# Kernel optimization log

Hardware: AMD Instinct MI355X
Metric: run time of the kernel (lower is better)

Reference implementation:

```python
import jax, jax.numpy as jnp
import numpy as np

GRID_SIZE, SPLINE_ORDER = 5, 3
NUM_BASES = GRID_SIZE + SPLINE_ORDER  # 8
GRID = jnp.asarray(np.arange(-SPLINE_ORDER, GRID_SIZE + SPLINE_ORDER + 1, dtype=np.float32) * (2.0 / GRID_SIZE) - 1.0)  # (12,)


def _b_splines(x):
    # x: (M, F) -> (M, F, NUM_BASES), Cox-de Boor recursion on shared uniform grid
    g = GRID
    xe = x[..., None]
    b = ((xe >= g[:-1]) & (xe < g[1:])).astype(x.dtype)
    for k in range(1, SPLINE_ORDER + 1):
        b = ((xe - g[:-(k + 1)]) / (g[k:-1] - g[:-(k + 1)]) * b[..., :-1]
             + (g[k + 1:] - xe) / (g[k + 1:] - g[1:-k]) * b[..., 1:])
    return b


def _kan_linear(x, base_w, spline_w):
    # x: (M, Fin); base_w: (Fout, Fin); spline_w: (Fout, Fin, NUM_BASES)
    base = jax.nn.silu(x) @ base_w.T
    spl = _b_splines(x).reshape(x.shape[0], -1) @ spline_w.reshape(spline_w.shape[0], -1).T
    return base + spl


def _ln(x, g, b, eps=1e-5):
    mu = jnp.mean(x, -1, keepdims=True)
    var = jnp.var(x, -1, keepdims=True)
    return (x - mu) * jax.lax.rsqrt(var + eps) * g + b


def _dwconv(img, w, b):
    C = img.shape[1]
    out = jax.lax.conv_general_dilated(img, w, (1, 1), 'SAME',
        dimension_numbers=('NCHW', 'OIHW', 'NCHW'), feature_group_count=C)
    return out + b[None, :, None, None]


def _dw_bn_relu(x, H, W, w, b, gamma, beta, eps=1e-5):
    # BN in eval mode with running_mean=0, running_var=1
    B, N, C = x.shape
    img = x.transpose(0, 2, 1).reshape(B, C, H, W)
    out = _dwconv(img, w, b)
    out = out * (gamma * (1.0 / np.sqrt(1.0 + eps)))[None, :, None, None] + beta[None, :, None, None]
    out = jax.nn.relu(out)
    return out.reshape(B, C, H * W).transpose(0, 2, 1)


def _cross_selective_scan(img, x_proj_w, dt_w, dt_b, A_logs, Ds, g, b):
    # img: (B, Di, H, W). 4-direction diagonal/antidiagonal selective scan (VMamba-style).
    B, Di, H, W = img.shape
    L = H * W
    K = x_proj_w.shape[0]
    R = dt_w.shape[2]
    Nst = A_logs.shape[1]
    i = jnp.arange(H)[:, None]
    j = jnp.arange(W)[None, :]
    diag = (i + j) % W
    adiag = (j - i) % W
    diag_inv = (jnp.arange(W)[None, :] - i) % W
    adiag_inv = (jnp.arange(W)[None, :] + i) % W

    def gather(x, idx):
        gth = jnp.take_along_axis(x, idx[None, None], axis=3)  # (B,Di,H,W)
        return gth.transpose(0, 1, 3, 2).reshape(B, Di, L)

    def scatter(flat, idx_inv):
        v = flat.reshape(B, Di, W, H).transpose(0, 1, 3, 2)
        return jnp.take_along_axis(v, idx_inv[None, None], axis=3)

    gd, gad = gather(img, diag), gather(img, adiag)
    xs = jnp.stack([gd, gad, jnp.flip(gd, -1), jnp.flip(gad, -1)], axis=1)  # (B,K,Di,L)
    x_dbl = jnp.einsum('bkdl,kcd->bkcl', xs, x_proj_w)
    dts, Bs, Cs = jnp.split(x_dbl, [R, R + Nst], axis=2)  # (B,K,R,L),(B,K,N,L),(B,K,N,L)
    dts = jnp.einsum('bkrl,kdr->bkdl', dts, dt_w)
    delta = jax.nn.softplus(dts + dt_b[None, :, :, None])  # (B,K,Di,L)
    A = -jnp.exp(A_logs).reshape(K, Di, Nst)

    def step(hst, inp):
        u_t, d_t, B_t, C_t = inp  # (B,K,Di),(B,K,Di),(B,K,N),(B,K,N)
        dA = jnp.exp(d_t[..., None] * A)
        hst = dA * hst + (d_t * u_t)[..., None] * B_t[:, :, None, :]
        return hst, jnp.einsum('bkdn,bkn->bkd', hst, C_t)

    h0 = jnp.zeros((B, K, Di, Nst), img.dtype)
    _, ys = jax.lax.scan(step, h0,
        (xs.transpose(3, 0, 1, 2), delta.transpose(3, 0, 1, 2),
         Bs.transpose(3, 0, 1, 2), Cs.transpose(3, 0, 1, 2)))  # ys: (L,B,K,Di)
    ys = ys.transpose(1, 2, 3, 0) + Ds.reshape(K, Di)[None, :, :, None] * xs  # (B,K,Di,L)
    yd = ys[:, 0] + jnp.flip(ys[:, 2], -1)
    ya = ys[:, 1] + jnp.flip(ys[:, 3], -1)
    y = scatter(yd, diag_inv) + scatter(ya, adiag_inv)  # (B,Di,H,W)
    y = y.reshape(B, Di, L).transpose(0, 2, 1)
    return _ln(y, g, b)  # (B,L,Di)


def setup_inputs():
    key = jax.random.key(0)
    ks = iter(jax.random.split(key, 48))
    B, H, W, C = 4, 64, 64, 96
    Di, K, Nst = 2 * C, 4, 16
    R = int(np.ceil(C / 16))
    L = H * W

    def rn(shape, s=0.05):
        return jax.random.normal(next(ks), shape, jnp.float32) * s

    return dict(
        x=jax.random.normal(next(ks), (B, L, C), jnp.float32),
        H=H, W=W,
        norm1_g=jnp.ones((C,), jnp.float32), norm1_b=jnp.zeros((C,), jnp.float32),
        in_proj_w=rn((2 * Di, C)),
        conv_w=rn((Di, 1, 3, 3), 0.2), conv_b=jnp.zeros((Di,), jnp.float32),
        x_proj_w=rn((K, R + 2 * Nst, Di)),
        dt_w=rn((K, Di, R), 0.1), dt_b=rn((K, Di), 0.1),
        A_logs=jax.random.uniform(next(ks), (K * Di, Nst), jnp.float32),
        Ds=jnp.ones((K * Di,), jnp.float32),
        out_norm_g=jnp.ones((Di,), jnp.float32), out_norm_b=jnp.zeros((Di,), jnp.float32),
        out_proj_w=rn((C, Di)),
        norm2_g=jnp.ones((C,), jnp.float32), norm2_b=jnp.zeros((C,), jnp.float32),
        fc1_base_w=rn((C, C)), fc1_spline_w=rn((C, C, NUM_BASES), 0.02),
        fc2_base_w=rn((C, C)), fc2_spline_w=rn((C, C, NUM_BASES), 0.02),
        fc3_base_w=rn((C, C)), fc3_spline_w=rn((C, C, NUM_BASES), 0.02),
        dw1_w=rn((C, 1, 3, 3), 0.2), dw1_b=jnp.zeros((C,), jnp.float32),
        dw1_g=jnp.ones((C,), jnp.float32), dw1_beta=jnp.zeros((C,), jnp.float32),
        dw2_w=rn((C, 1, 3, 3), 0.2), dw2_b=jnp.zeros((C,), jnp.float32),
        dw2_g=jnp.ones((C,), jnp.float32), dw2_beta=jnp.zeros((C,), jnp.float32),
        dw3_w=rn((C, 1, 3, 3), 0.2), dw3_b=jnp.zeros((C,), jnp.float32),
        dw3_g=jnp.ones((C,), jnp.float32), dw3_beta=jnp.zeros((C,), jnp.float32),
    )


def reference(x, H, W, norm1_g, norm1_b, in_proj_w, conv_w, conv_b, x_proj_w,
              dt_w, dt_b, A_logs, Ds, out_norm_g, out_norm_b, out_proj_w,
              norm2_g, norm2_b, fc1_base_w, fc1_spline_w, fc2_base_w, fc2_spline_w,
              fc3_base_w, fc3_spline_w, dw1_w, dw1_b, dw1_g, dw1_beta,
              dw2_w, dw2_b, dw2_g, dw2_beta, dw3_w, dw3_b, dw3_g, dw3_beta):
    B, L, C = x.shape
    # --- SS2D branch ---
    h = _ln(x, norm1_g, norm1_b)
    xz = h @ in_proj_w.T  # (B,L,2*Di)
    Di = xz.shape[-1] // 2
    xin, z = xz[..., :Di], xz[..., Di:]
    img = xin.transpose(0, 2, 1).reshape(B, Di, H, W)
    img = jax.nn.silu(_dwconv(img, conv_w, conv_b))
    y = _cross_selective_scan(img, x_proj_w, dt_w, dt_b, A_logs, Ds, out_norm_g, out_norm_b)
    y = y * jax.nn.silu(z)
    x = x + y @ out_proj_w.T
    # --- KAN branch ---
    h = _ln(x, norm2_g, norm2_b)
    M = B * L
    t = _kan_linear(h.reshape(M, C), fc1_base_w, fc1_spline_w).reshape(B, L, -1)
    t = _dw_bn_relu(t, H, W, dw1_w, dw1_b, dw1_g, dw1_beta)
    t = _kan_linear(t.reshape(M, -1), fc2_base_w, fc2_spline_w).reshape(B, L, -1)
    t = _dw_bn_relu(t, H, W, dw2_w, dw2_b, dw2_g, dw2_beta)
    t = _kan_linear(t.reshape(M, -1), fc3_base_w, fc3_spline_w).reshape(B, L, -1)
    t = _dw_bn_relu(t, H, W, dw3_w, dw3_b, dw3_g, dw3_beta)
    return x + t
```

## Files before the change

### kernel.cpp

```cpp
#include <hip/hip_runtime.h>
#include <math.h>

constexpr int B_  = 4;
constexpr int H_  = 64;
constexpr int W_  = 64;
constexpr int C_  = 96;
constexpr int L_  = H_ * W_;
constexpr int DI  = 192;
constexpr int K_  = 4;
constexpr int NST = 16;
constexpr int R_  = 6;
constexpr int M_  = B_ * L_;

constexpr int NCH = 128;
constexpr int CL  = 32;
constexpr int DG  = 12;

constexpr int KANK = 864;
constexpr int KLAY = 96 * KANK;

typedef __attribute__((ext_vector_type(8))) short short8;
typedef __attribute__((ext_vector_type(4))) float floatx4;
typedef __attribute__((ext_vector_type(4))) unsigned short ushort4v;

__device__ __forceinline__ float wave_sum64(float v) {
#pragma unroll
  for (int off = 1; off < 64; off <<= 1) v += __shfl_xor(v, off, 64);
  return v;
}

__device__ __forceinline__ float exp2_hw(float x) {
  return __builtin_amdgcn_exp2f(x);
}

__device__ __forceinline__ int pos_kl(int k, int l) {
  int ll = (k >= 2) ? (L_ - 1 - l) : l;
  int i = ll & 63;
  int j = ll >> 6;
  int col = ((k & 1) == 0) ? ((i + j) & 63) : ((j - i) & 63);
  return (i << 6) + col;
}

__device__ __forceinline__ int pos_pair(int pr, int ll) {
  int i = ll & 63, j = ll >> 6;
  int col = (pr == 0) ? ((i + j) & 63) : ((j - i) & 63);
  return (i << 6) + col;
}

__device__ __forceinline__ float silu_f(float x) {
  return x / (1.f + __expf(-x));
}

__device__ __forceinline__ float softplus_fast(float s) {
  return fmaxf(s, 0.f) + __logf(1.f + __expf(-fabsf(s)));
}

__device__ __forceinline__ unsigned short f2bf(float f) {
  unsigned u = __float_as_uint(f);
  unsigned r = (u + 0x7FFFu + ((u >> 16) & 1u)) >> 16;
  return (unsigned short)r;
}

__device__ __forceinline__ float bf2f(unsigned short h) {
  return __uint_as_float(((unsigned)h) << 16);
}

__device__ __forceinline__ void spline8(float x, float* bb ) {
#pragma unroll
  for (int i2 = 0; i2 < 11; i2++) {
    float g0 = 0.4f * i2 - 2.2f;
    float g1 = 0.4f * i2 - 1.8f;
    bb[i2] = (x >= g0 && x < g1) ? 1.f : 0.f;
  }
#pragma unroll
  for (int k2 = 1; k2 <= 3; k2++) {
    float invd = 1.f / (0.4f * k2);
#pragma unroll
    for (int i2 = 0; i2 + k2 < 11; i2++) {
      float gi   = 0.4f * i2 - 2.2f;
      float gik1 = 0.4f * (i2 + k2 + 1) - 2.2f;
      bb[i2] = (x - gi) * invd * bb[i2] + (gik1 - x) * invd * bb[i2 + 1];
    }
  }
}

__global__ __launch_bounds__(256) void ln96_kernel(const float* __restrict__ in,
    const float* __restrict__ g, const float* __restrict__ b,
    float* __restrict__ out) {
  int wave = blockIdx.x * 4 + (threadIdx.x >> 6);
  int lane = threadIdx.x & 63;
  const float* rp = in + (size_t)wave * C_;
  float v0 = rp[lane];
  float v1 = (lane < C_ - 64) ? rp[lane + 64] : 0.f;
  float s  = wave_sum64(v0 + v1);
  float s2 = wave_sum64(v0 * v0 + v1 * v1);
  float mean = s * (1.f / C_);
  float var  = s2 * (1.f / C_) - mean * mean;
  float inv  = rsqrtf(var + 1e-5f);
  float* op = out + (size_t)wave * C_;
  op[lane] = (v0 - mean) * inv * g[lane] + b[lane];
  if (lane < C_ - 64) op[lane + 64] = (v1 - mean) * inv * g[lane + 64] + b[lane + 64];
}

__global__ __launch_bounds__(256) void prep_inproj_kernel(const float* __restrict__ w,
    unsigned short* __restrict__ wio) {
  int idx = blockIdx.x * 256 + threadIdx.x;
  if (idx >= 384 * 96) return;
  float v = w[idx];
  unsigned short hh = f2bf(v);
  wio[idx] = hh;
  wio[36864 + idx] = f2bf(v - bf2f(hh));
}

__global__ __launch_bounds__(256) void prep_outproj_kernel(const float* __restrict__ w,
    unsigned short* __restrict__ wo) {
  int idx = blockIdx.x * 256 + threadIdx.x;
  if (idx >= 96 * 192) return;
  float v = w[idx];
  unsigned short hh = f2bf(v);
  wo[idx] = hh;
  wo[18432 + idx] = f2bf(v - bf2f(hh));
}

__global__ __launch_bounds__(256) void prep_a2_kernel(const float* __restrict__ A_logs,
    float* __restrict__ a2g) {
  int idx = blockIdx.x * 256 + threadIdx.x;
  if (idx < K_ * DI * NST) a2g[idx] = -__expf(A_logs[idx]) * 1.44269504f;
}

__global__ __launch_bounds__(256) void gemm_in_mfma_kernel(const float* __restrict__ h,
    const unsigned short* __restrict__ wio, float* __restrict__ xin,
    float* __restrict__ z) {
  __shared__ __align__(16) unsigned short Wh[96][104];
  __shared__ __align__(16) unsigned short Wl[96][104];
  int row0 = (blockIdx.x >> 1) * 64;
  int nc0  = (blockIdx.x & 1) * 2;
  int tid = threadIdx.x;
  int wv = tid >> 6, lane = tid & 63, mrow = lane & 15, quad = lane >> 4;

  short8 ah[3], al[3];
  const float* hr = h + (size_t)(row0 + wv * 16 + mrow) * C_;
#pragma unroll
  for (int ks = 0; ks < 3; ks++) {
    float4 va = *(const float4*)&hr[ks * 32 + quad * 8];
    float4 vb = *(const float4*)&hr[ks * 32 + quad * 8 + 4];
    float f[8] = {va.x, va.y, va.z, va.w, vb.x, vb.y, vb.z, vb.w};
    short8 hh, ll;
#pragma unroll
    for (int q = 0; q < 8; q++) {
      unsigned short hv = f2bf(f[q]);
      hh[q] = (short)hv;
      ll[q] = (short)f2bf(f[q] - bf2f(hv));
    }
    ah[ks] = hh; al[ks] = ll;
  }
  for (int nci = 0; nci < 2; nci++) {
    int nc = nc0 + nci;
    if (nci) __syncthreads();
    for (int t = tid; t < 96 * 12; t += 256) {
      int j = t / 12, u = t % 12;
      *(short8*)&Wh[j][u * 8] = *(const short8*)&wio[(size_t)(nc * 96 + j) * 96 + u * 8];
      *(short8*)&Wl[j][u * 8] = *(const short8*)&wio[(size_t)(384 + nc * 96 + j) * 96 + u * 8];
    }
    __syncthreads();
    floatx4 acc[6];
#pragma unroll
    for (int q = 0; q < 6; q++) acc[q] = (floatx4)(0.f);
#pragma unroll
    for (int ks = 0; ks < 3; ks++) {
#pragma unroll
      for (int nt = 0; nt < 6; nt++) {
        short8 bh = *(const short8*)&Wh[nt * 16 + mrow][ks * 32 + quad * 8];
        short8 bl = *(const short8*)&Wl[nt * 16 + mrow][ks * 32 + quad * 8];
        acc[nt] = __builtin_amdgcn_mfma_f32_16x16x32_bf16(ah[ks], bh, acc[nt], 0, 0, 0);
        acc[nt] = __builtin_amdgcn_mfma_f32_16x16x32_bf16(al[ks], bh, acc[nt], 0, 0, 0);
        acc[nt] = __builtin_amdgcn_mfma_f32_16x16x32_bf16(ah[ks], bl, acc[nt], 0, 0, 0);
      }
    }
#pragma unroll
    for (int nt = 0; nt < 6; nt++) {
      int j = nc * 96 + nt * 16 + mrow;
#pragma unroll
      for (int rg = 0; rg < 4; rg++) {
        int row = row0 + wv * 16 + quad * 4 + rg;
        float v = acc[nt][rg];
        if (j < DI) xin[(size_t)row * DI + j] = v;
        else        z[(size_t)row * DI + (j - DI)] = v;
      }
    }
  }
}

__global__ __launch_bounds__(192) void conv_silu_kernel(const float* __restrict__ xin,
    const float* __restrict__ cw, const float* __restrict__ cb, float* __restrict__ imgT) {
  int p0 = blockIdx.x * 2;
  int b = p0 >> 12;
  int ij = p0 & 4095;
  int i = ij >> 6, j0 = ij & 63;
  int c = threadIdx.x;
  float v[3][4];
#pragma unroll
  for (int r = 0; r < 3; r++) {
    int ii = i - 1 + r;
    bool rok = (ii >= 0 && ii < H_);
#pragma unroll
    for (int cc = 0; cc < 4; cc++) {
      int jj = j0 - 1 + cc;
      v[r][cc] = (rok && jj >= 0 && jj < W_)
                     ? xin[((size_t)b * L_ + ii * W_ + jj) * DI + c] : 0.f;
    }
  }
  const float* wc = cw + c * 9;
  float w[9];
#pragma unroll
  for (int q = 0; q < 9; q++) w[q] = wc[q];
  float a0 = cb[c], a1 = a0;
#pragma unroll
  for (int r = 0; r < 3; r++) {
#pragma unroll
    for (int t = 0; t < 3; t++) {
      a0 += v[r][t]     * w[r * 3 + t];
      a1 += v[r][t + 1] * w[r * 3 + t];
    }
  }
  imgT[(size_t)p0 * DI + c]       = silu_f(a0);
  imgT[(size_t)(p0 + 1) * DI + c] = silu_f(a1);
}

__global__ __launch_bounds__(256) void xdbl_mfma_kernel(const float* __restrict__ imgT,
    const float* __restrict__ xpw, float* __restrict__ dts_g,
    float* __restrict__ BsT, float* __restrict__ CsT) {
  __shared__ __align__(16) unsigned short Ah[64][104];
  __shared__ __align__(16) unsigned short Al[64][104];
  __shared__ __align__(16) unsigned short Wh[48][104];
  __shared__ __align__(16) unsigned short Wl[48][104];
  __shared__ int pos_s[64];

  int blk = blockIdx.x;
  int lt = blk & 63;
  int bk = blk >> 6;
  int k = bk % K_, b = bk / K_;
  int l0 = lt * 64;
  int tid = threadIdx.x;
  int wid = tid >> 6;
  int lane = tid & 63;
  int mrow = lane & 15, quad = lane >> 4;

  if (tid < 64) pos_s[tid] = pos_kl(k, l0 + tid);
  __syncthreads();

  floatx4 acc[3];
#pragma unroll
  for (int q = 0; q < 3; q++) acc[q] = (floatx4)(0.f);

  const float* img_b = imgT + (size_t)b * L_ * DI;

  for (int kc = 0; kc < 2; kc++) {
    if (kc) __syncthreads();
    for (int t = tid; t < 64 * 24; t += 256) {
      int li = t / 24, c4 = (t % 24) * 4;
      const float4 v = *(const float4*)&img_b[(size_t)pos_s[li] * DI + kc * 96 + c4];
      ushort4v h4, l4;
      float fv[4] = {v.x, v.y, v.z, v.w};
#pragma unroll
      for (int q = 0; q < 4; q++) {
        unsigned short hh = f2bf(fv[q]);
        h4[q] = hh;
        l4[q] = f2bf(fv[q] - bf2f(hh));
      }
      *(ushort4v*)&Ah[li][c4] = h4;
      *(ushort4v*)&Al[li][c4] = l4;
    }
    for (int t = tid; t < 48 * 24; t += 256) {
      int j = t / 24, c4 = (t % 24) * 4;
      ushort4v h4 = (ushort4v)0, l4 = (ushort4v)0;
      if (j < 38) {
        int c = (j < 32) ? (j + 6) : (j - 32);
        const float4 v = *(const float4*)&xpw[((size_t)(k * 38 + c)) * DI + kc * 96 + c4];
        float fv[4] = {v.x, v.y, v.z, v.w};
#pragma unroll
        for (int q = 0; q < 4; q++) {
          unsigned short hh = f2bf(fv[q]);
          h4[q] = hh;
          l4[q] = f2bf(fv[q] - bf2f(hh));
        }
      }
      *(ushort4v*)&Wh[j][c4] = h4;
      *(ushort4v*)&Wl[j][c4] = l4;
    }
    __syncthreads();
#pragma unroll
    for (int ks = 0; ks < 3; ks++) {
      short8 ah = *(const short8*)&Ah[wid * 16 + mrow][ks * 32 + quad * 8];
      short8 al = *(const short8*)&Al[wid * 16 + mrow][ks * 32 + quad * 8];
#pragma unroll
      for (int nt = 0; nt < 3; nt++) {
        short8 bh = *(const short8*)&Wh[nt * 16 + mrow][ks * 32 + quad * 8];
        short8 bl = *(const short8*)&Wl[nt * 16 + mrow][ks * 32 + quad * 8];
        acc[nt] = __builtin_amdgcn_mfma_f32_16x16x32_bf16(ah, bh, acc[nt], 0, 0, 0);
        acc[nt] = __builtin_amdgcn_mfma_f32_16x16x32_bf16(al, bh, acc[nt], 0, 0, 0);
        acc[nt] = __builtin_amdgcn_mfma_f32_16x16x32_bf16(ah, bl, acc[nt], 0, 0, 0);
      }
    }
  }
  size_t bkL = (size_t)(b * K_ + k) * L_ + l0;
#pragma unroll
  for (int rg = 0; rg < 4; rg++) {
    int grow = wid * 16 + quad * 4 + rg;
    size_t base = (bkL + grow) * NST;
    BsT[base + mrow] = acc[0][rg];
    CsT[base + mrow] = acc[1][rg];
    if (mrow < R_) dts_g[(bkL + grow) * 8 + mrow] = acc[2][rg];
  }
}

__global__ __launch_bounds__(192) void scan1_kernel(const float* __restrict__ imgT,
    const float* __restrict__ dts_g, const float* __restrict__ BsT,
    const float* __restrict__ a2g, const float* __restrict__ dtw,
    const float* __restrict__ dtb, float* __restrict__ hend,
    float* __restrict__ aprod) {
  __shared__ float bs_s[CL][NST];
  __shared__ float dt_s[CL][8];
  int blk = blockIdx.x;
  int c = blk % NCH;
  int tmp = blk / NCH;
  int k = tmp % K_, b = tmp / K_;
  int l0 = c * CL;
  int d = threadIdx.x;
  const float* img_b = imgT + (size_t)b * L_ * DI;
  {
    const float* Bs_bk = BsT + ((size_t)(b * K_ + k) * L_ + l0) * NST;
    for (int t = d; t < CL * NST; t += 192) bs_s[t >> 4][t & 15] = Bs_bk[t];
    const float* Dt = dts_g + ((size_t)(b * K_ + k) * L_ + l0) * 8;
    for (int t = d; t < CL * 8; t += 192) dt_s[t >> 3][t & 7] = Dt[t];
  }
  float A2[NST];
  {
    const floatx4* ap = (const floatx4*)(a2g + (size_t)(k * DI + d) * NST);
#pragma unroll
    for (int i = 0; i < 4; i++) {
      floatx4 v = ap[i];
      A2[4 * i] = v[0]; A2[4 * i + 1] = v[1]; A2[4 * i + 2] = v[2]; A2[4 * i + 3] = v[3];
    }
  }
  float w6[6], bias;
  {
    const float* wp = dtw + ((size_t)k * DI + d) * R_;
#pragma unroll
    for (int r = 0; r < 6; r++) w6[r] = wp[r];
    bias = dtb[k * DI + d];
  }
  float u[CL];
#pragma unroll
  for (int q = 0; q < CL; q++)
    u[q] = img_b[(size_t)pos_kl(k, l0 + q) * DI + d];
  __syncthreads();
  float dc[CL];
  float sum_dlt = 0.f;
#pragma unroll
  for (int q = 0; q < CL; q++) {
    const floatx4* dp = (const floatx4*)&dt_s[q][0];
    floatx4 d0 = dp[0], d1 = dp[1];
    float s = bias + w6[0] * d0[0] + w6[1] * d0[1] + w6[2] * d0[2]
                   + w6[3] * d0[3] + w6[4] * d1[0] + w6[5] * d1[1];
    dc[q] = softplus_fast(s);
    sum_dlt += dc[q];
  }
  float h[NST];
#pragma unroll
  for (int n = 0; n < NST; n++) h[n] = 0.f;
#pragma unroll
  for (int q = 0; q < CL; q++) {
    float du = dc[q] * u[q];
    floatx4 bsv[4];
    const floatx4* bp = (const floatx4*)&bs_s[q][0];
#pragma unroll
    for (int i = 0; i < 4; i++) bsv[i] = bp[i];
#pragma unroll
    for (int n = 0; n < NST; n++) {
      float dA = exp2_hw(dc[q] * A2[n]);
      h[n] = dA * h[n] + du * bsv[n >> 2][n & 3];
    }
  }
  size_t base = ((size_t)(b * K_ + k) * NCH + c) * (DI * NST) + d;
#pragma unroll
  for (int n = 0; n < NST; n++) {
    hend[base + (size_t)n * DI]  = h[n];
    aprod[base + (size_t)n * DI] = exp2_hw(A2[n] * sum_dlt);
  }
}

__global__ __launch_bounds__(256) void scan_carry_kernel(float* __restrict__ hend,
    const float* __restrict__ aprod) {
  constexpr int PF = 8;
  int blk = blockIdx.x;
  int part = blk % DG;
  int bk = blk / DG;
  const size_t DNS = (size_t)DI * NST;
  size_t base = (size_t)bk * NCH * DNS + (size_t)part * 256 + threadIdx.x;
  float hb[PF], ab[PF];
#pragma unroll
  for (int q = 0; q < PF; q++) {
    hb[q] = hend[base + (size_t)q * DNS];
    ab[q] = aprod[base + (size_t)q * DNS];
  }
  float carry = 0.f;
  for (int c0 = 0; c0 < NCH; c0 += PF) {
    float hn[PF], an[PF];
    if (c0 + PF < NCH) {
#pragma unroll
      for (int q = 0; q < PF; q++) {
        hn[q] = hend[base + (size_t)(c0 + PF + q) * DNS];
        an[q] = aprod[base + (size_t)(c0 + PF + q) * DNS];
      }
    } else {
#pragma unroll
      for (int q = 0; q < PF; q++) { hn[q] = 0.f; an[q] = 0.f; }
    }
#pragma unroll
    for (int q = 0; q < PF; q++) {
      hend[base + (size_t)(c0 + q) * DNS] = carry;
      carry = ab[q] * carry + hb[q];
    }
#pragma unroll
    for (int q = 0; q < PF; q++) { hb[q] = hn[q]; ab[q] = an[q]; }
  }
}

__global__ __launch_bounds__(192) void scan2_pair_kernel(const float* __restrict__ imgT,
    const float* __restrict__ dts_g, const float* __restrict__ BsT,
    const float* __restrict__ CsT, const float* __restrict__ a2g,
    const float* __restrict__ dtw, const float* __restrict__ dtb,
    const float* __restrict__ Ds, const float* __restrict__ carry_in,
    float* __restrict__ y02, float* __restrict__ y13) {
  __shared__ float bsf[CL][NST], csf[CL][NST], bsr[CL][NST], csr[CL][NST];
  __shared__ float dtf[CL][8], dtr[CL][8];
  __shared__ float y_lds[CL][DI];
  int blk = blockIdx.x;
  int c  = blk % NCH;
  int pr = (blk / NCH) & 1;
  int b  = blk / (2 * NCH);
  int kf = pr, kr = pr + 2;
  int p0 = c * CL;
  int d = threadIdx.x;
  const float* img_b = imgT + (size_t)b * L_ * DI;
  {
    const float* Bf = BsT + ((size_t)(b * K_ + kf) * L_ + p0) * NST;
    const float* Cf = CsT + ((size_t)(b * K_ + kf) * L_ + p0) * NST;
    for (int t = d; t < CL * NST; t += 192) {
      bsf[t >> 4][t & 15] = Bf[t];
      csf[t >> 4][t & 15] = Cf[t];
    }
    const float* Br = BsT + (size_t)(b * K_ + kr) * L_ * NST;
    const float* Cr = CsT + (size_t)(b * K_ + kr) * L_ * NST;
    for (int t = d; t < CL * NST; t += 192) {
      int q = t >> 4, n = t & 15;
      size_t sr = (size_t)(L_ - 1 - p0 - q) * NST + n;
      bsr[q][n] = Br[sr];
      csr[q][n] = Cr[sr];
    }
    const float* Df = dts_g + ((size_t)(b * K_ + kf) * L_ + p0) * 8;
    for (int t = d; t < CL * 8; t += 192) dtf[t >> 3][t & 7] = Df[t];
    const float* Dr = dts_g + (size_t)(b * K_ + kr) * L_ * 8;
    for (int t = d; t < CL * 8; t += 192) {
      int q = t >> 3, r = t & 7;
      dtr[q][r] = Dr[(size_t)(L_ - 1 - p0 - q) * 8 + r];
    }
  }
  float u[CL];
#pragma unroll
  for (int q = 0; q < CL; q++)
    u[q] = img_b[(size_t)pos_pair(pr, p0 + q) * DI + d];
  float dsum = 0.f;
  if (pr == 0) dsum = Ds[d] + Ds[DI + d] + Ds[2 * DI + d] + Ds[3 * DI + d];
  __syncthreads();
  float A2[NST], h[NST], w6[6], bias, dc[CL];
  {
    const floatx4* ap = (const floatx4*)(a2g + (size_t)(kf * DI + d) * NST);
#pragma unroll
    for (int i = 0; i < 4; i++) {
      floatx4 v = ap[i];
      A2[4 * i] = v[0]; A2[4 * i + 1] = v[1]; A2[4 * i + 2] = v[2]; A2[4 * i + 3] = v[3];
    }
    size_t cb = ((size_t)(b * K_ + kf) * NCH + c) * (DI * NST) + d;
#pragma unroll
    for (int n = 0; n < NST; n++) h[n] = carry_in[cb + (size_t)n * DI];
    const float* wp = dtw + ((size_t)kf * DI + d) * R_;
#pragma unroll
    for (int r = 0; r < 6; r++) w6[r] = wp[r];
    bias = dtb[kf * DI + d];
  }
#pragma unroll
  for (int q = 0; q < CL; q++) {
    const floatx4* dp = (const floatx4*)&dtf[q][0];
    floatx4 d0 = dp[0], d1 = dp[1];
    float s = bias + w6[0] * d0[0] + w6[1] * d0[1] + w6[2] * d0[2]
                   + w6[3] * d0[3] + w6[4] * d1[0] + w6[5] * d1[1];
    dc[q] = softplus_fast(s);
  }
#pragma unroll
  for (int q = 0; q < CL; q++) {
    float du = dc[q] * u[q];
    floatx4 bsv[4], csv[4];
    const floatx4* bp = (const floatx4*)&bsf[q][0];
    const floatx4* cp = (const floatx4*)&csf[q][0];
#pragma unroll
    for (int i = 0; i < 4; i++) { bsv[i] = bp[i]; csv[i] = cp[i]; }
    float yq = dsum * u[q];
#pragma unroll
    for (int n = 0; n < NST; n++) {
      float dA = exp2_hw(dc[q] * A2[n]);
      h[n] = dA * h[n] + du * bsv[n >> 2][n & 3];
      yq += h[n] * csv[n >> 2][n & 3];
    }
    y_lds[q][d] = yq;
  }
  {
    const floatx4* ap = (const floatx4*)(a2g + (size_t)(kr * DI + d) * NST);
#pragma unroll
    for (int i = 0; i < 4; i++) {
      floatx4 v = ap[i];
      A2[4 * i] = v[0]; A2[4 * i + 1] = v[1]; A2[4 * i + 2] = v[2]; A2[4 * i + 3] = v[3];
    }
    size_t cb = ((size_t)(b * K_ + kr) * NCH + (NCH - 1 - c)) * (DI * NST) + d;
#pragma unroll
    for (int n = 0; n < NST; n++) h[n] = carry_in[cb + (size_t)n * DI];
    const float* wp = dtw + ((size_t)kr * DI + d) * R_;
#pragma unroll
    for (int r = 0; r < 6; r++) w6[r] = wp[r];
    bias = dtb[kr * DI + d];
  }
#pragma unroll
  for (int q = 0; q < CL; q++) {
    const floatx4* dp = (const floatx4*)&dtr[q][0];
    floatx4 d0 = dp[0], d1 = dp[1];
    float s = bias + w6[0] * d0[0] + w6[1] * d0[1] + w6[2] * d0[2]
                   + w6[3] * d0[3] + w6[4] * d1[0] + w6[5] * d1[1];
    dc[q] = softplus_fast(s);
  }
  float* yout = (pr == 0) ? y02 : y13;
#pragma unroll
  for (int qq = 0; qq < CL; qq++) {
    int q = CL - 1 - qq;
    float du = dc[q] * u[q];
    floatx4 bsv[4], csv[4];
    const floatx4* bp = (const floatx4*)&bsr[q][0];
    const floatx4* cp = (const floatx4*)&csr[q][0];
#pragma unroll
    for (int i = 0; i < 4; i++) { bsv[i] = bp[i]; csv[i] = cp[i]; }
    float yq = y_lds[q][d];
#pragma unroll
    for (int n = 0; n < NST; n++) {
      float dA = exp2_hw(dc[q] * A2[n]);
      h[n] = dA * h[n] + du * bsv[n >> 2][n & 3];
      yq += h[n] * csv[n >> 2][n & 3];
    }
    yout[((size_t)b * L_ + pos_pair(pr, p0 + q)) * DI + d] = yq;
  }
}

__global__ __launch_bounds__(256) void ln_mulz_kernel(const float* __restrict__ y02,
    const float* __restrict__ y13, const float* __restrict__ g,
    const float* __restrict__ bb, float* __restrict__ z) {
  int wave = blockIdx.x * 4 + (threadIdx.x >> 6);
  int lane = threadIdx.x & 63;
  const float* rp = y02 + (size_t)wave * DI;
  const float* rq = y13 + (size_t)wave * DI;
  float v0 = rp[lane]       + rq[lane];
  float v1 = rp[lane + 64]  + rq[lane + 64];
  float v2 = rp[lane + 128] + rq[lane + 128];
  float s  = wave_sum64(v0 + v1 + v2);
  float s2 = wave_sum64(v0 * v0 + v1 * v1 + v2 * v2);
  float mean = s * (1.f / DI);
  float var  = s2 * (1.f / DI) - mean * mean;
  float inv  = rsqrtf(var + 1e-5f);
  float* zp = z + (size_t)wave * DI;
  float vv[3] = {v0, v1, v2};
#pragma unroll
  for (int q = 0; q < 3; q++) {
    int c = lane + 64 * q;
    float zv = zp[c];
    zp[c] = ((vv[q] - mean) * inv * g[c] + bb[c]) * silu_f(zv);
  }
}

__global__ __launch_bounds__(256) void outproj_mfma_kernel(const float* __restrict__ yz,
    const unsigned short* __restrict__ wo, const float* __restrict__ x,
    float* __restrict__ x_res) {
  __shared__ __align__(16) unsigned short Wh[96][104];
  __shared__ __align__(16) unsigned short Wl[96][104];
  int row0 = blockIdx.x * 64;
  int tid = threadIdx.x;
  int wv = tid >> 6, lane = tid & 63, mrow = lane & 15, quad = lane >> 4;

  floatx4 acc[6];
#pragma unroll
  for (int q = 0; q < 6; q++) acc[q] = (floatx4)(0.f);

  const float* yr = yz + (size_t)(row0 + wv * 16 + mrow) * DI;
  for (int kc = 0; kc < 2; kc++) {
    if (kc) __syncthreads();
    for (int t = tid; t < 96 * 12; t += 256) {
      int j = t / 12, u = t % 12;
      *(short8*)&Wh[j][u * 8] = *(const short8*)&wo[(size_t)j * DI + kc * 96 + u * 8];
      *(short8*)&Wl[j][u * 8] = *(const short8*)&wo[18432 + (size_t)j * DI + kc * 96 + u * 8];
    }
    __syncthreads();
#pragma unroll
    for (int ks = 0; ks < 3; ks++) {
      float4 va = *(const float4*)&yr[kc * 96 + ks * 32 + quad * 8];
      float4 vb = *(const float4*)&yr[kc * 96 + ks * 32 + quad * 8 + 4];
      float f[8] = {va.x, va.y, va.z, va.w, vb.x, vb.y, vb.z, vb.w};
      short8 ah, al;
#pragma unroll
      for (int q = 0; q < 8; q++) {
        unsigned short hv = f2bf(f[q]);
        ah[q] = (short)hv;
        al[q] = (short)f2bf(f[q] - bf2f(hv));
      }
#pragma unroll
      for (int nt = 0; nt < 6; nt++) {
        short8 bh = *(const short8*)&Wh[nt * 16 + mrow][ks * 32 + quad * 8];
        short8 bl = *(const short8*)&Wl[nt * 16 + mrow][ks * 32 + quad * 8];
        acc[nt] = __builtin_amdgcn_mfma_f32_16x16x32_bf16(ah, bh, acc[nt], 0, 0, 0);
        acc[nt] = __builtin_amdgcn_mfma_f32_16x16x32_bf16(al, bh, acc[nt], 0, 0, 0);
        acc[nt] = __builtin_amdgcn_mfma_f32_16x16x32_bf16(ah, bl, acc[nt], 0, 0, 0);
      }
    }
  }
#pragma unroll
  for (int nt = 0; nt < 6; nt++) {
    int j = nt * 16 + mrow;
#pragma unroll
    for (int rg = 0; rg < 4; rg++) {
      int row = row0 + wv * 16 + quad * 4 + rg;
      x_res[(size_t)row * C_ + j] = x[(size_t)row * C_ + j] + acc[nt][rg];
    }
  }
}

__global__ __launch_bounds__(256) void prepw_kernel(const float* __restrict__ bw1,
    const float* __restrict__ sw1, const float* __restrict__ bw2,
    const float* __restrict__ sw2, const float* __restrict__ bw3,
    const float* __restrict__ sw3, unsigned short* __restrict__ wcat) {
  int idx = blockIdx.x * 256 + threadIdx.x;
  if (idx >= 3 * KLAY) return;
  int layer = idx / KLAY, rem = idx % KLAY;
  int j = rem / KANK, k = rem % KANK;
  const float* bw = (layer == 0) ? bw1 : (layer == 1) ? bw2 : bw3;
  const float* sw = (layer == 0) ? sw1 : (layer == 1) ? sw2 : sw3;
  float v = (k < C_) ? bw[j * C_ + k] : sw[j * 768 + (k - C_)];
  wcat[idx] = f2bf(v);
}

__global__ __launch_bounds__(256) void kan_mfma_kernel(const float* __restrict__ in,
    const unsigned short* __restrict__ wl, float* __restrict__ out) {
  __shared__ __align__(16) float x_s[32][100];
  __shared__ __align__(16) unsigned short A_s[32][104];
  __shared__ __align__(16) unsigned short W_s[96][104];
  int row0 = blockIdx.x * 32;
  int tid = threadIdx.x;
  for (int t = tid; t < 32 * 24; t += 256) {
    int r = t / 24, c4 = (t % 24) * 4;
    *(float4*)&x_s[r][c4] = *(const float4*)&in[(size_t)(row0 + r) * C_ + c4];
  }
  floatx4 acc[3];
#pragma unroll
  for (int q = 0; q < 3; q++) acc[q] = (floatx4)(0.f);
  int wv = tid >> 6;
  int rh = wv >> 1, ch = wv & 1;
  int lane = tid & 63;
  int mrow = lane & 15, quad = lane >> 4;
  __syncthreads();
  for (int ci = 0; ci < 9; ci++) {
    if (ci) __syncthreads();
    for (int t = tid; t < 96 * 12; t += 256) {
      int j = t / 12, u = t % 12;
      *(short8*)&W_s[j][u * 8] =
          *(const short8*)&wl[(size_t)j * KANK + ci * 96 + u * 8];
    }
    if (ci == 0) {
      for (int t = tid; t < 32 * 48; t += 256) {
        int r = t / 48, k2 = (t % 48) * 2;
        unsigned v = (unsigned)f2bf(silu_f(x_s[r][k2])) |
                     ((unsigned)f2bf(silu_f(x_s[r][k2 + 1])) << 16);
        *(unsigned*)&A_s[r][k2] = v;
      }
    } else {
      int c0 = (ci - 1) * 12;
      for (int t = tid; t < 32 * 12; t += 256) {
        int r = t & 31, cl = t >> 5;
        float x = x_s[r][c0 + cl];
        float bb[11];
        spline8(x, bb);
        short8 av;
#pragma unroll
        for (int q = 0; q < 8; q++) av[q] = (short)f2bf(bb[q]);
        *(short8*)&A_s[r][cl * 8] = av;
      }
    }
    __syncthreads();
#pragma unroll
    for (int ks = 0; ks < 3; ks++) {
      short8 a = *(const short8*)&A_s[rh * 16 + mrow][ks * 32 + quad * 8];
#pragma unroll
      for (int ct = 0; ct < 3; ct++) {
        short8 b = *(const short8*)&W_s[ch * 48 + ct * 16 + mrow][ks * 32 + quad * 8];
        acc[ct] = __builtin_amdgcn_mfma_f32_16x16x32_bf16(a, b, acc[ct], 0, 0, 0);
      }
    }
  }
#pragma unroll
  for (int ct = 0; ct < 3; ct++)
#pragma unroll
    for (int rg = 0; rg < 4; rg++) {
      int row = row0 + rh * 16 + quad * 4 + rg;
      out[(size_t)row * C_ + ch * 48 + ct * 16 + mrow] = acc[ct][rg];
    }
}

__global__ __launch_bounds__(192) void dwbn_kernel(const float* __restrict__ t,
    const float* __restrict__ w, const float* __restrict__ bias,
    const float* __restrict__ gamma, const float* __restrict__ beta,
    const float* __restrict__ addres, float* __restrict__ out) {
  int tid = threadIdx.x;
  int half = (tid >= 96) ? 1 : 0;
  int c = tid - half * 96;
  int p0 = blockIdx.x * 4 + half * 2;
  int b = p0 >> 12;
  int ij = p0 & 4095;
  int i = ij >> 6, j0 = ij & 63;
  float v[3][4];
#pragma unroll
  for (int r = 0; r < 3; r++) {
    int ii = i - 1 + r;
    bool rok = (ii >= 0 && ii < H_);
#pragma unroll
    for (int cc = 0; cc < 4; cc++) {
      int jj = j0 - 1 + cc;
      v[r][cc] = (rok && jj >= 0 && jj < W_)
                     ? t[((size_t)b * L_ + ii * W_ + jj) * C_ + c] : 0.f;
    }
  }
  const float* wc = w + c * 9;
  float wv[9];
#pragma unroll
  for (int q = 0; q < 9; q++) wv[q] = wc[q];
  float a0 = bias[c], a1 = a0;
#pragma unroll
  for (int r = 0; r < 3; r++) {
#pragma unroll
    for (int tt = 0; tt < 3; tt++) {
      a0 += v[r][tt]     * wv[r * 3 + tt];
      a1 += v[r][tt + 1] * wv[r * 3 + tt];
    }
  }
  float gsc = gamma[c] * rsqrtf(1.f + 1e-5f);
  float bt = beta[c];
  float o0 = fmaxf(a0 * gsc + bt, 0.f);
  float o1 = fmaxf(a1 * gsc + bt, 0.f);
  if (addres != nullptr) {
    o0 += addres[(size_t)p0 * C_ + c];
    o1 += addres[(size_t)(p0 + 1) * C_ + c];
  }
  out[(size_t)p0 * C_ + c]       = o0;
  out[(size_t)(p0 + 1) * C_ + c] = o1;
}

extern "C" void kernel_launch(void* const* d_in, const int* in_sizes, int n_in,
                              void* d_out, int out_size, void* d_ws, size_t ws_size,
                              hipStream_t stream) {
  const float* x         = (const float*)d_in[0];
  const float* norm1_g   = (const float*)d_in[3];
  const float* norm1_b   = (const float*)d_in[4];
  const float* in_proj_w = (const float*)d_in[5];
  const float* conv_w    = (const float*)d_in[6];
  const float* conv_b    = (const float*)d_in[7];
  const float* x_proj_w  = (const float*)d_in[8];
  const float* dt_w      = (const float*)d_in[9];
  const float* dt_b      = (const float*)d_in[10];
  const float* A_logs    = (const float*)d_in[11];
  const float* Ds        = (const float*)d_in[12];
  const float* out_ng    = (const float*)d_in[13];
  const float* out_nb    = (const float*)d_in[14];
  const float* out_proj_w= (const float*)d_in[15];
  const float* norm2_g   = (const float*)d_in[16];
  const float* norm2_b   = (const float*)d_in[17];
  const float* fc1_bw    = (const float*)d_in[18];
  const float* fc1_sw    = (const float*)d_in[19];
  const float* fc2_bw    = (const float*)d_in[20];
  const float* fc2_sw    = (const float*)d_in[21];
  const float* fc3_bw    = (const float*)d_in[22];
  const float* fc3_sw    = (const float*)d_in[23];
  const float* dw1_w     = (const float*)d_in[24];
  const float* dw1_b     = (const float*)d_in[25];
  const float* dw1_g     = (const float*)d_in[26];
  const float* dw1_be    = (const float*)d_in[27];
  const float* dw2_w     = (const float*)d_in[28];
  const float* dw2_b     = (const float*)d_in[29];
  const float* dw2_g     = (const float*)d_in[30];
  const float* dw2_be    = (const float*)d_in[31];
  const float* dw3_w     = (const float*)d_in[32];
  const float* dw3_b     = (const float*)d_in[33];
  const float* dw3_g     = (const float*)d_in[34];
  const float* dw3_be    = (const float*)d_in[35];

  float* ws = (float*)d_ws;
  float* h_buf   = ws;
  float* xin_buf = h_buf + (size_t)M_ * C_;
  float* z_buf   = xin_buf + (size_t)M_ * DI;
  float* imgT    = z_buf + (size_t)M_ * DI;
  float* BsT     = imgT + (size_t)M_ * DI;
  float* CsT     = BsT + (size_t)B_ * K_ * L_ * NST;
  float* y_pre   = CsT + (size_t)B_ * K_ * L_ * NST;
  float* x_res   = y_pre + (size_t)M_ * DI;
  float* t_a     = x_res + (size_t)M_ * C_;
  float* t_b     = t_a + (size_t)M_ * C_;
  float* hend    = t_b + (size_t)M_ * C_;
  float* aprod   = hend + (size_t)B_ * K_ * NCH * DI * NST;
  float* a2_buf  = aprod + (size_t)B_ * K_ * NCH * DI * NST;
  float* dts_g   = t_a;
  unsigned short* wio  = (unsigned short*)t_b;
  unsigned short* wo_p = wio + 2 * 36864;
  float* y13     = xin_buf;
  unsigned short* wcat = (unsigned short*)BsT;

  ln96_kernel<<<M_ / 4, 256, 0, stream>>>(x, norm1_g, norm1_b, h_buf);
  prep_inproj_kernel<<<144, 256, 0, stream>>>(in_proj_w, wio);
  prep_outproj_kernel<<<72, 256, 0, stream>>>(out_proj_w, wo_p);
  prep_a2_kernel<<<48, 256, 0, stream>>>(A_logs, a2_buf);
  gemm_in_mfma_kernel<<<(M_ / 64) * 2, 256, 0, stream>>>(h_buf, wio, xin_buf, z_buf);
  conv_silu_kernel<<<M_ / 2, 192, 0, stream>>>(xin_buf, conv_w, conv_b, imgT);
  xdbl_mfma_kernel<<<B_ * K_ * (L_ / 64), 256, 0, stream>>>(imgT, x_proj_w, dts_g,
                                                            BsT, CsT);
  scan1_kernel<<<B_ * K_ * NCH, 192, 0, stream>>>(imgT, dts_g, BsT, a2_buf,
                                                  dt_w, dt_b, hend, aprod);
  scan_carry_kernel<<<B_ * K_ * DG, 256, 0, stream>>>(hend, aprod);
  scan2_pair_kernel<<<B_ * 2 * NCH, 192, 0, stream>>>(imgT, dts_g, BsT, CsT, a2_buf,
                                                      dt_w, dt_b, Ds, hend,
                                                      y_pre, y13);
  prepw_kernel<<<(3 * KLAY + 255) / 256, 256, 0, stream>>>(fc1_bw, fc1_sw, fc2_bw,
                                                           fc2_sw, fc3_bw, fc3_sw, wcat);
  ln_mulz_kernel<<<M_ / 4, 256, 0, stream>>>(y_pre, y13, out_ng, out_nb, z_buf);
  outproj_mfma_kernel<<<M_ / 64, 256, 0, stream>>>(z_buf, wo_p, x, x_res);
  ln96_kernel<<<M_ / 4, 256, 0, stream>>>(x_res, norm2_g, norm2_b, h_buf);
  kan_mfma_kernel<<<M_ / 32, 256, 0, stream>>>(h_buf, wcat, t_a);
  dwbn_kernel<<<M_ / 4, 192, 0, stream>>>(t_a, dw1_w, dw1_b, dw1_g, dw1_be, nullptr, t_b);
  kan_mfma_kernel<<<M_ / 32, 256, 0, stream>>>(t_b, wcat + KLAY, t_a);
  dwbn_kernel<<<M_ / 4, 192, 0, stream>>>(t_a, dw2_w, dw2_b, dw2_g, dw2_be, nullptr, t_b);
  kan_mfma_kernel<<<M_ / 32, 256, 0, stream>>>(t_b, wcat + 2 * KLAY, t_a);
  dwbn_kernel<<<M_ / 4, 192, 0, stream>>>(t_a, dw3_w, dw3_b, dw3_g, dw3_be, x_res, (float*)d_out);
}
```

Baseline: 422.0 us.

## Fuse out-norm LayerNorm and gating into out-proj GEMM; recompute chunk decay in carry

Two changes. First, the separate LayerNorm-times-silu(z) kernel is folded into the out-projection MFMA kernel. Each block now stages its 64 rows of y in LDS, computes the row statistics, applies the gate and feeds the GEMM from LDS, which removes a full write and read of the intermediate z activation. Second, scan1 no longer writes a per-(d,n) chunk decay product. It stores only the per-chunk delta sum, and the carry kernel recomputes exp2(A*sum) itself, cutting that tensor's traffic by a factor of 16. The costs are a large LDS footprint (about 90KB per block), which may limit occupancy, and some extra exp work in the carry kernel.

```diff
diff --git a/kernel.cpp b/kernel.cpp
--- a/kernel.cpp
+++ b/kernel.cpp
@@ -318,7 +318,7 @@
     const float* __restrict__ dts_g, const float* __restrict__ BsT,
     const float* __restrict__ a2g, const float* __restrict__ dtw,
     const float* __restrict__ dtb, float* __restrict__ hend,
-    float* __restrict__ aprod) {
+    float* __restrict__ sdl) {
   __shared__ float bs_s[CL][NST];
   __shared__ float dt_s[CL][8];
   int blk = blockIdx.x;
@@ -384,25 +384,30 @@
   }
   size_t base = ((size_t)(b * K_ + k) * NCH + c) * (DI * NST) + d;
 #pragma unroll
-  for (int n = 0; n < NST; n++) {
-    hend[base + (size_t)n * DI]  = h[n];
-    aprod[base + (size_t)n * DI] = exp2_hw(A2[n] * sum_dlt);
-  }
+  for (int n = 0; n < NST; n++)
+    hend[base + (size_t)n * DI] = h[n];
+  sdl[((size_t)(b * K_ + k) * NCH + c) * DI + d] = sum_dlt;
 }
 
 __global__ __launch_bounds__(256) void scan_carry_kernel(float* __restrict__ hend,
-    const float* __restrict__ aprod) {
+    const float* __restrict__ sdl, const float* __restrict__ a2g) {
   constexpr int PF = 8;
   int blk = blockIdx.x;
   int part = blk % DG;
   int bk = blk / DG;
+  int k = bk % K_;
   const size_t DNS = (size_t)DI * NST;
-  size_t base = (size_t)bk * NCH * DNS + (size_t)part * 256 + threadIdx.x;
+  int idx = part * 256 + threadIdx.x;
+  int n = idx / DI;
+  int d = idx - n * DI;
+  float a2 = a2g[(size_t)(k * DI + d) * NST + n];
+  size_t base  = (size_t)bk * NCH * DNS + idx;
+  size_t sbase = (size_t)bk * NCH * DI + d;
   float hb[PF], ab[PF];
 #pragma unroll
   for (int q = 0; q < PF; q++) {
     hb[q] = hend[base + (size_t)q * DNS];
-    ab[q] = aprod[base + (size_t)q * DNS];
+    ab[q] = exp2_hw(a2 * sdl[sbase + (size_t)q * DI]);
   }
   float carry = 0.f;
   for (int c0 = 0; c0 < NCH; c0 += PF) {
@@ -411,7 +416,7 @@
 #pragma unroll
       for (int q = 0; q < PF; q++) {
         hn[q] = hend[base + (size_t)(c0 + PF + q) * DNS];
-        an[q] = aprod[base + (size_t)(c0 + PF + q) * DNS];
+        an[q] = exp2_hw(a2 * sdl[sbase + (size_t)(c0 + PF + q) * DI]);
       }
     } else {
 #pragma unroll
@@ -559,45 +564,52 @@
   }
 }
 
-__global__ __launch_bounds__(256) void ln_mulz_kernel(const float* __restrict__ y02,
-    const float* __restrict__ y13, const float* __restrict__ g,
-    const float* __restrict__ bb, float* __restrict__ z) {
-  int wave = blockIdx.x * 4 + (threadIdx.x >> 6);
-  int lane = threadIdx.x & 63;
-  const float* rp = y02 + (size_t)wave * DI;
-  const float* rq = y13 + (size_t)wave * DI;
-  float v0 = rp[lane]       + rq[lane];
-  float v1 = rp[lane + 64]  + rq[lane + 64];
-  float v2 = rp[lane + 128] + rq[lane + 128];
-  float s  = wave_sum64(v0 + v1 + v2);
-  float s2 = wave_sum64(v0 * v0 + v1 * v1 + v2 * v2);
-  float mean = s * (1.f / DI);
-  float var  = s2 * (1.f / DI) - mean * mean;
-  float inv  = rsqrtf(var + 1e-5f);
-  float* zp = z + (size_t)wave * DI;
-  float vv[3] = {v0, v1, v2};
-#pragma unroll
-  for (int q = 0; q < 3; q++) {
-    int c = lane + 64 * q;
-    float zv = zp[c];
-    zp[c] = ((vv[q] - mean) * inv * g[c] + bb[c]) * silu_f(zv);
-  }
-}
-
-__global__ __launch_bounds__(256) void outproj_mfma_kernel(const float* __restrict__ yz,
+__global__ __launch_bounds__(256) void lnz_outproj_kernel(const float* __restrict__ y02,
+    const float* __restrict__ y13, const float* __restrict__ lg,
+    const float* __restrict__ lb, const float* __restrict__ z,
     const unsigned short* __restrict__ wo, const float* __restrict__ x,
     float* __restrict__ x_res) {
   __shared__ __align__(16) unsigned short Wh[96][104];
   __shared__ __align__(16) unsigned short Wl[96][104];
+  __shared__ float zg[64][193];
+  __shared__ float stat_mean[64], stat_inv[64];
   int row0 = blockIdx.x * 64;
   int tid = threadIdx.x;
   int wv = tid >> 6, lane = tid & 63, mrow = lane & 15, quad = lane >> 4;
-
+  for (int t = tid; t < 64 * DI; t += 256) {
+    int r = t / DI, c = t - r * DI;
+    size_t gi = (size_t)(row0 + r) * DI + c;
+    zg[r][c] = y02[gi] + y13[gi];
+  }
+  __syncthreads();
+  {
+    int r = tid >> 2, part = tid & 3;
+    float s = 0.f, s2 = 0.f;
+#pragma unroll 4
+    for (int i = 0; i < 48; i++) {
+      float v = zg[r][part * 48 + i];
+      s += v; s2 += v * v;
+    }
+    s  += __shfl_xor(s, 1, 64);  s  += __shfl_xor(s, 2, 64);
+    s2 += __shfl_xor(s2, 1, 64); s2 += __shfl_xor(s2, 2, 64);
+    if (part == 0) {
+      float mean = s * (1.f / DI);
+      float var  = s2 * (1.f / DI) - mean * mean;
+      stat_mean[r] = mean;
+      stat_inv[r]  = rsqrtf(var + 1e-5f);
+    }
+  }
+  __syncthreads();
+  for (int t = tid; t < 64 * DI; t += 256) {
+    int r = t / DI, c = t - r * DI;
+    size_t gi = (size_t)(row0 + r) * DI + c;
+    float zv = z[gi];
+    zg[r][c] = ((zg[r][c] - stat_mean[r]) * stat_inv[r] * lg[c] + lb[c]) * silu_f(zv);
+  }
+  __syncthreads();
   floatx4 acc[6];
 #pragma unroll
   for (int q = 0; q < 6; q++) acc[q] = (floatx4)(0.f);
-
-  const float* yr = yz + (size_t)(row0 + wv * 16 + mrow) * DI;
   for (int kc = 0; kc < 2; kc++) {
     if (kc) __syncthreads();
     for (int t = tid; t < 96 * 12; t += 256) {
@@ -608,15 +620,14 @@
     __syncthreads();
 #pragma unroll
     for (int ks = 0; ks < 3; ks++) {
-      float4 va = *(const float4*)&yr[kc * 96 + ks * 32 + quad * 8];
-      float4 vb = *(const float4*)&yr[kc * 96 + ks * 32 + quad * 8 + 4];
-      float f[8] = {va.x, va.y, va.z, va.w, vb.x, vb.y, vb.z, vb.w};
+      const float* zr = &zg[wv * 16 + mrow][kc * 96 + ks * 32 + quad * 8];
       short8 ah, al;
 #pragma unroll
       for (int q = 0; q < 8; q++) {
-        unsigned short hv = f2bf(f[q]);
+        float f = zr[q];
+        unsigned short hv = f2bf(f);
         ah[q] = (short)hv;
-        al[q] = (short)f2bf(f[q] - bf2f(hv));
+        al[q] = (short)f2bf(f - bf2f(hv));
       }
 #pragma unroll
       for (int nt = 0; nt < 6; nt++) {
@@ -817,8 +828,8 @@
   float* t_a     = x_res + (size_t)M_ * C_;
   float* t_b     = t_a + (size_t)M_ * C_;
   float* hend    = t_b + (size_t)M_ * C_;
-  float* aprod   = hend + (size_t)B_ * K_ * NCH * DI * NST;
-  float* a2_buf  = aprod + (size_t)B_ * K_ * NCH * DI * NST;
+  float* sdl_buf = hend + (size_t)B_ * K_ * NCH * DI * NST;
+  float* a2_buf  = sdl_buf + (size_t)B_ * K_ * NCH * DI;
   float* dts_g   = t_a;
   unsigned short* wio  = (unsigned short*)t_b;
   unsigned short* wo_p = wio + 2 * 36864;
@@ -834,15 +845,15 @@
   xdbl_mfma_kernel<<<B_ * K_ * (L_ / 64), 256, 0, stream>>>(imgT, x_proj_w, dts_g,
                                                             BsT, CsT);
   scan1_kernel<<<B_ * K_ * NCH, 192, 0, stream>>>(imgT, dts_g, BsT, a2_buf,
-                                                  dt_w, dt_b, hend, aprod);
-  scan_carry_kernel<<<B_ * K_ * DG, 256, 0, stream>>>(hend, aprod);
+                                                  dt_w, dt_b, hend, sdl_buf);
+  scan_carry_kernel<<<B_ * K_ * DG, 256, 0, stream>>>(hend, sdl_buf, a2_buf);
   scan2_pair_kernel<<<B_ * 2 * NCH, 192, 0, stream>>>(imgT, dts_g, BsT, CsT, a2_buf,
                                                       dt_w, dt_b, Ds, hend,
                                                       y_pre, y13);
   prepw_kernel<<<(3 * KLAY + 255) / 256, 256, 0, stream>>>(fc1_bw, fc1_sw, fc2_bw,
                                                            fc2_sw, fc3_bw, fc3_sw, wcat);
-  ln_mulz_kernel<<<M_ / 4, 256, 0, stream>>>(y_pre, y13, out_ng, out_nb, z_buf);
-  outproj_mfma_kernel<<<M_ / 64, 256, 0, stream>>>(z_buf, wo_p, x, x_res);
+  lnz_outproj_kernel<<<M_ / 64, 256, 0, stream>>>(y_pre, y13, out_ng, out_nb,
+                                                  z_buf, wo_p, x, x_res);
   ln96_kernel<<<M_ / 4, 256, 0, stream>>>(x_res, norm2_g, norm2_b, h_buf);
   kan_mfma_kernel<<<M_ / 32, 256, 0, stream>>>(h_buf, wcat, t_a);
   dwbn_kernel<<<M_ / 4, 192, 0, stream>>>(t_a, dw1_w, dw1_b, dw1_g, dw1_be, nullptr, t_b);
```

Result: no change. 429.4 us (+1.7%).
